# Performance work log

Measured on AMD Instinct MI355X. Metric: run time of the kernel, lower is better.

Reference implementation:

```python
import jax, jax.numpy as jnp
import numpy as np

T, D, H, E = 8192, 1024, 512, 8
BLK = 32  # MXFP8 scaling block size along the contraction dim


def setup_inputs() -> dict:
    key = jax.random.key(0)
    k1, k2, k3, k4 = jax.random.split(key, 4)
    # qdata: values representable-ish in e4m3 (we use small normal floats)
    output_e4m3 = jax.random.normal(k1, (T, D), dtype=jnp.float32)
    # e8m0 scales are powers of two, one per 32-element block along dim
    output_scales_e8m0 = jnp.exp2(
        jax.random.randint(k2, (T, D // BLK), -2, 3).astype(jnp.float32)
    )
    # uniform token distribution across experts (tokens are expert-contiguous)
    num_tokens_per_expert = jnp.full((E,), T // E, dtype=jnp.int32)
    expert_padded_offsets = jnp.zeros((E,), dtype=jnp.int32)  # unused by forward body
    w13 = jax.random.normal(k3, (E, 2 * H, D), dtype=jnp.float32) * 0.02
    w2 = jax.random.normal(k4, (E, D, H), dtype=jnp.float32) * 0.02
    return {
        "output_e4m3": output_e4m3,
        "output_scales_e8m0": output_scales_e8m0,
        "num_tokens_per_expert": num_tokens_per_expert,
        "expert_padded_offsets": expert_padded_offsets,
        "w13": w13,
        "w2": w2,
    }


def reference(output_e4m3, output_scales_e8m0, num_tokens_per_expert,
              expert_padded_offsets, w13, w2):
    # Dequantize MXFP8: qdata * per-block e8m0 scale, blocks of 32 along dim.
    scales = jnp.repeat(output_scales_e8m0, BLK, axis=-1)  # [T, D]
    x = output_e4m3 * scales  # [T, D] high-precision reference activations
    # Grouped GEMM 1: tokens are expert-contiguous with uniform group sizes,
    # so the ragged grouped matmul reduces to a batched einsum per expert.
    tpe = T // E
    xg = x.reshape(E, tpe, D)                       # [E, tpe, D]
    h13 = jnp.einsum("etd,ehd->eth", xg, w13)       # [E, tpe, 2H]
    h1, h3 = h13[..., :H], h13[..., H:]
    h = jax.nn.silu(h1) * h3                        # fused SiLU-gate
    # Grouped GEMM 2
    out = jnp.einsum("eth,edh->etd", h, w2)         # [E, tpe, D]
    return out.reshape(T, D)
```

## Files before the change

### kernel.cpp

```cpp
#include <hip/hip_runtime.h>
#include <hip/hip_bf16.h>

#define T_TOK 8192
#define DDIM  1024
#define HDIM  512
#define NE    8
#define TPE   (T_TOK / NE)

typedef __attribute__((ext_vector_type(4))) float floatx4;
typedef __attribute__((ext_vector_type(8))) short bf16x8;

__device__ __forceinline__ unsigned short f2bf(float f) {
    union { float f; unsigned int u; } v;
    v.f = f;
    unsigned int u = v.u;
    unsigned int r = u + 0x7FFFu + ((u >> 16) & 1u);
    return (unsigned short)(r >> 16);
}

__device__ __forceinline__ unsigned int cvt_pk_bf16(float lo, float hi) {
    unsigned int r;
    asm("v_cvt_pk_bf16_f32 %0, %1, %2" : "=v"(r) : "v"(lo), "v"(hi));
    return r;
}

__device__ __forceinline__ void gld_lds16(const void* g, void* l) {
    __builtin_amdgcn_global_load_lds(
        (const __attribute__((address_space(1))) unsigned int*)g,
        (__attribute__((address_space(3))) unsigned int*)l, 16, 0, 0);
}

__global__ __launch_bounds__(256)
void convert_x_kernel(const float* __restrict__ X, const float* __restrict__ S,
                      unsigned short* __restrict__ Xb)
{
    const int NTX = (T_TOK * DDIM) / 4;
    const int stride = gridDim.x * blockDim.x;
    for (int i = blockIdx.x * blockDim.x + threadIdx.x; i < NTX; i += stride) {
        int row = i >> 8;
        int c4  = i & 255;
        float4 v = reinterpret_cast<const float4*>(X)[i];
        float sc = S[row * (DDIM / 32) + (c4 >> 3)];
        ushort4 b;
        b.x = f2bf(v.x * sc); b.y = f2bf(v.y * sc);
        b.z = f2bf(v.z * sc); b.w = f2bf(v.w * sc);
        reinterpret_cast<ushort4*>(Xb)[i] = b;
    }
}

__device__ __forceinline__ int xcd_swizzle_512(int raw) {
    return (raw & 7) * 64 + (raw >> 3);
}


__global__ __launch_bounds__(256, 2)
void gemm1_silu_kernel(const unsigned short* __restrict__ Xb,
                       const float* __restrict__ W13,
                       __hip_bfloat16* __restrict__ Hout)
{
    const int bid = xcd_swizzle_512(blockIdx.x);
    const int e  = bid >> 6;
    const int mt = (bid >> 3) & 7;
    const int nt = bid & 7;
    const int tok0 = e * TPE + mt * 128;
    const float* __restrict__ We = W13 + (size_t)e * (2 * HDIM) * DDIM;

    __shared__ __hip_bfloat16 sA[2][128][64];
    __shared__ __hip_bfloat16 sB[2][128][64];

    const int tid  = threadIdx.x;
    const int lane = tid & 63;
    const int wave = tid >> 6;
    const int wr = wave >> 1;
    const int wc = wave & 1;
    const int lr = lane & 15;
    const int sw0 = ((lane >> 4) ^ (lane & 7));

    floatx4 acc1[4][2] = {};
    floatx4 acc3[4][2] = {};

    const int srow0 = (tid >> 3);
    const int c8    = (tid & 7) * 8;
    const int dcol  = (tid & 7) * 8;
    const int gcol  = ((tid & 7) ^ (srow0 & 7)) * 8;
    const int swcol = gcol;

    float4 rB0[8], rB1[8];

    auto LOADB = [&](int kk, float4* rB) {
        const int k0 = kk * 64;
        #pragma unroll
        for (int j = 0; j < 4; ++j) {
            int row = srow0 + j * 32;
            int wrow = (j < 2) ? (nt * 64 + row)
                               : (HDIM + nt * 64 + (row - 64));
            const float* p = &We[(size_t)wrow * DDIM + k0 + c8];
            rB[2*j]   = *reinterpret_cast<const float4*>(p);
            rB[2*j+1] = *reinterpret_cast<const float4*>(p + 4);
        }
    };
    auto STAGEA = [&](int kk, int buf) {
        const int k0 = kk * 64;
        #pragma unroll
        for (int j = 0; j < 4; ++j) {
            int row = srow0 + j * 32;
            gld_lds16(&Xb[(size_t)(tok0 + row) * DDIM + k0 + gcol],
                      &sA[buf][row][dcol]);
        }
    };
    auto WRITEB = [&](int buf, const float4* rB) {
        #pragma unroll
        for (int j = 0; j < 4; ++j) {
            int row = srow0 + j * 32;
            uint4 w;
            w.x = cvt_pk_bf16(rB[2*j].x,   rB[2*j].y);
            w.y = cvt_pk_bf16(rB[2*j].z,   rB[2*j].w);
            w.z = cvt_pk_bf16(rB[2*j+1].x, rB[2*j+1].y);
            w.w = cvt_pk_bf16(rB[2*j+1].z, rB[2*j+1].w);
            *reinterpret_cast<uint4*>(&sB[buf][row][swcol]) = w;
        }
    };
    auto COMPUTE = [&](int buf) {
        #pragma unroll
        for (int ks = 0; ks < 2; ++ks) {
            const int rc = (sw0 ^ (ks << 2)) << 3;
            bf16x8 a[4], b1[2], b3[2];
            #pragma unroll
            for (int m = 0; m < 4; ++m)
                a[m] = *reinterpret_cast<const bf16x8*>(&sA[buf][wr * 64 + m * 16 + lr][rc]);
            #pragma unroll
            for (int n = 0; n < 2; ++n) {
                b1[n] = *reinterpret_cast<const bf16x8*>(&sB[buf][wc * 32 + n * 16 + lr][rc]);
                b3[n] = *reinterpret_cast<const bf16x8*>(&sB[buf][64 + wc * 32 + n * 16 + lr][rc]);
            }
            #pragma unroll
            for (int m = 0; m < 4; ++m)
                #pragma unroll
                for (int n = 0; n < 2; ++n) {
                    acc1[m][n] = __builtin_amdgcn_mfma_f32_16x16x32_bf16(a[m], b1[n], acc1[m][n], 0, 0, 0);
                    acc3[m][n] = __builtin_amdgcn_mfma_f32_16x16x32_bf16(a[m], b3[n], acc3[m][n], 0, 0, 0);
                }
        }
    };

    LOADB(0, rB0);
    __builtin_amdgcn_sched_barrier(0);
    LOADB(1, rB1);
    __builtin_amdgcn_sched_barrier(0);
    STAGEA(0, 0);
    __builtin_amdgcn_sched_barrier(0);
    asm volatile("s_waitcnt vmcnt(12)" ::: "memory");
    __builtin_amdgcn_sched_barrier(0);

    for (int t = 0; t < DDIM / 64 - 2; t += 2) {
        WRITEB(0, rB0);
        __builtin_amdgcn_sched_barrier(0);
        LOADB(t + 2, rB0);
        __builtin_amdgcn_sched_barrier(0);
        STAGEA(t + 1, 1);
        __builtin_amdgcn_sched_barrier(0);
        asm volatile("s_waitcnt vmcnt(12) lgkmcnt(0)" ::: "memory");
        __builtin_amdgcn_sched_barrier(0);
        __builtin_amdgcn_s_barrier();
        COMPUTE(0);
        __builtin_amdgcn_s_barrier();
        WRITEB(1, rB1);
        __builtin_amdgcn_sched_barrier(0);
        LOADB(t + 3, rB1);
        __builtin_amdgcn_sched_barrier(0);
        STAGEA(t + 2, 0);
        __builtin_amdgcn_sched_barrier(0);
        asm volatile("s_waitcnt vmcnt(12) lgkmcnt(0)" ::: "memory");
        __builtin_amdgcn_sched_barrier(0);
        __builtin_amdgcn_s_barrier();
        COMPUTE(1);
        __builtin_amdgcn_s_barrier();
    }

    WRITEB(0, rB0);
    __builtin_amdgcn_sched_barrier(0);
    STAGEA(15, 1);
    __builtin_amdgcn_sched_barrier(0);
    asm volatile("s_waitcnt vmcnt(4) lgkmcnt(0)" ::: "memory");
    __builtin_amdgcn_sched_barrier(0);
    __builtin_amdgcn_s_barrier();
    COMPUTE(0);
    __builtin_amdgcn_s_barrier();
    WRITEB(1, rB1);
    __builtin_amdgcn_sched_barrier(0);
    asm volatile("s_waitcnt vmcnt(0) lgkmcnt(0)" ::: "memory");
    __builtin_amdgcn_sched_barrier(0);
    __builtin_amdgcn_s_barrier();
    COMPUTE(1);

    const int hcol0 = nt * 64 + wc * 32;
    #pragma unroll
    for (int m = 0; m < 4; ++m) {
        #pragma unroll
        for (int n = 0; n < 2; ++n) {
            #pragma unroll
            for (int i = 0; i < 4; ++i) {
                int row = tok0 + wr * 64 + m * 16 + (lane >> 4) * 4 + i;
                int col = hcol0 + n * 16 + (lane & 15);
                float h1 = acc1[m][n][i];
                float h3 = acc3[m][n][i];
                float sig = 1.0f / (1.0f + __expf(-h1));
                Hout[(size_t)row * HDIM + col] = __float2bfloat16(h1 * sig * h3);
            }
        }
    }
}

__global__ __launch_bounds__(256, 2)
void gemm2_kernel(const __hip_bfloat16* __restrict__ Hin,
                  const float* __restrict__ W2,
                  float* __restrict__ Out)
{
    const int bid = xcd_swizzle_512(blockIdx.x);
    const int e  = bid >> 6;
    const int nt = (bid >> 3) & 7;
    const int mt = bid & 7;
    const int tok0 = e * TPE + mt * 128;
    const float* __restrict__ We = W2 + (size_t)e * DDIM * HDIM;

    __shared__ __hip_bfloat16 sA[2][128][64];
    __shared__ __hip_bfloat16 sB[2][128][64];

    const int tid  = threadIdx.x;
    const int lane = tid & 63;
    const int wave = tid >> 6;
    const int wr = wave >> 1;
    const int wc = wave & 1;
    const int lr = lane & 15;
    const int sw0 = ((lane >> 4) ^ (lane & 7));

    floatx4 acc[4][4] = {};

    const int srow0 = (tid >> 3);
    const int c8    = (tid & 7) * 8;
    const int dcol  = (tid & 7) * 8;
    const int swcol = ((tid & 7) ^ (srow0 & 7)) * 8;

    float4 rB[8];

    auto LOADB = [&](int kk) {
        const int k0 = kk * 64;
        #pragma unroll
        for (int j = 0; j < 4; ++j) {
            int row = srow0 + j * 32;
            const float* p = &We[(size_t)(nt * 128 + row) * HDIM + k0 + c8];
            rB[2*j]   = *reinterpret_cast<const float4*>(p);
            rB[2*j+1] = *reinterpret_cast<const float4*>(p + 4);
        }
    };
    auto STAGEA = [&](int kk, int buf) {
        const int k0 = kk * 64;
        #pragma unroll
        for (int j = 0; j < 4; ++j) {
            int row = srow0 + j * 32;
            gld_lds16(&Hin[(size_t)(tok0 + row) * HDIM + k0 + swcol],
                      &sA[buf][row][dcol]);
        }
    };
    auto WRITEB = [&](int buf) {
        #pragma unroll
        for (int j = 0; j < 4; ++j) {
            int row = srow0 + j * 32;
            uint4 w;
            w.x = cvt_pk_bf16(rB[2*j].x,   rB[2*j].y);
            w.y = cvt_pk_bf16(rB[2*j].z,   rB[2*j].w);
            w.z = cvt_pk_bf16(rB[2*j+1].x, rB[2*j+1].y);
            w.w = cvt_pk_bf16(rB[2*j+1].z, rB[2*j+1].w);
            *reinterpret_cast<uint4*>(&sB[buf][row][swcol]) = w;
        }
    };
    auto COMPUTE = [&](int buf) {
        #pragma unroll
        for (int ks = 0; ks < 2; ++ks) {
            const int rc = (sw0 ^ (ks << 2)) << 3;
            bf16x8 a[4], b[4];
            #pragma unroll
            for (int m = 0; m < 4; ++m)
                a[m] = *reinterpret_cast<const bf16x8*>(&sA[buf][wr * 64 + m * 16 + lr][rc]);
            #pragma unroll
            for (int n = 0; n < 4; ++n)
                b[n] = *reinterpret_cast<const bf16x8*>(&sB[buf][wc * 64 + n * 16 + lr][rc]);
            #pragma unroll
            for (int m = 0; m < 4; ++m)
                #pragma unroll
                for (int n = 0; n < 4; ++n)
                    acc[m][n] = __builtin_amdgcn_mfma_f32_16x16x32_bf16(a[m], b[n], acc[m][n], 0, 0, 0);
        }
    };

    LOADB(0);
    __builtin_amdgcn_sched_barrier(0);
    STAGEA(0, 0);
    __builtin_amdgcn_sched_barrier(0);
    for (int kk = 0; kk < HDIM / 64 - 1; ++kk) {
        const int buf = kk & 1;
        asm volatile("s_waitcnt vmcnt(4)" ::: "memory");
        __builtin_amdgcn_sched_barrier(0);
        WRITEB(buf);
        __builtin_amdgcn_sched_barrier(0);
        LOADB(kk + 1);
        __builtin_amdgcn_sched_barrier(0);
        STAGEA(kk + 1, buf ^ 1);
        __builtin_amdgcn_sched_barrier(0);
        asm volatile("s_waitcnt vmcnt(12) lgkmcnt(0)" ::: "memory");
        __builtin_amdgcn_sched_barrier(0);
        __builtin_amdgcn_s_barrier();
        COMPUTE(buf);
        __builtin_amdgcn_s_barrier();
    }
    asm volatile("s_waitcnt vmcnt(4)" ::: "memory");
    __builtin_amdgcn_sched_barrier(0);
    WRITEB(1);
    asm volatile("s_waitcnt vmcnt(0) lgkmcnt(0)" ::: "memory");
    __builtin_amdgcn_sched_barrier(0);
    __builtin_amdgcn_s_barrier();
    COMPUTE(1);

    const int dcol0 = nt * 128 + wc * 64;
    #pragma unroll
    for (int m = 0; m < 4; ++m) {
        #pragma unroll
        for (int n = 0; n < 4; ++n) {
            #pragma unroll
            for (int i = 0; i < 4; ++i) {
                int row = tok0 + wr * 64 + m * 16 + (lane >> 4) * 4 + i;
                int col = dcol0 + n * 16 + (lane & 15);
                Out[(size_t)row * DDIM + col] = acc[m][n][i];
            }
        }
    }
}

extern "C" void kernel_launch(void* const* d_in, const int* in_sizes, int n_in,
                              void* d_out, int out_size, void* d_ws, size_t ws_size,
                              hipStream_t stream) {
    const float* X   = (const float*)d_in[0];
    const float* S   = (const float*)d_in[1];
    const float* W13 = (const float*)d_in[4];
    const float* W2  = (const float*)d_in[5];
    float* Out = (float*)d_out;

    __hip_bfloat16* Hb = (__hip_bfloat16*)d_ws;
    unsigned short* Xb = (unsigned short*)d_out;

    convert_x_kernel<<<2048, 256, 0, stream>>>(X, S, Xb);
    gemm1_silu_kernel<<<NE * 8 * 8, 256, 0, stream>>>(Xb, W13, Hb);
    gemm2_kernel<<<NE * 8 * 8, 256, 0, stream>>>(Hb, W2, Out);
}
```

Measured before the change: 56.11 us.

## Restructure GEMM1 main loop to overlap next-tile loads with MFMA compute

```diff
diff --git a/kernel.cpp b/kernel.cpp
--- a/kernel.cpp
+++ b/kernel.cpp
@@ -9,6 +9,8 @@
 
 typedef __attribute__((ext_vector_type(4))) float floatx4;
 typedef __attribute__((ext_vector_type(8))) short bf16x8;
+
+#define SBAR() __builtin_amdgcn_sched_barrier(0)
 
 __device__ __forceinline__ unsigned short f2bf(float f) {
     union { float f; unsigned int u; } v;
@@ -120,78 +122,70 @@
             *reinterpret_cast<uint4*>(&sB[buf][row][swcol]) = w;
         }
     };
-    auto COMPUTE = [&](int buf) {
-        #pragma unroll
-        for (int ks = 0; ks < 2; ++ks) {
-            const int rc = (sw0 ^ (ks << 2)) << 3;
-            bf16x8 a[4], b1[2], b3[2];
-            #pragma unroll
-            for (int m = 0; m < 4; ++m)
-                a[m] = *reinterpret_cast<const bf16x8*>(&sA[buf][wr * 64 + m * 16 + lr][rc]);
+    auto COMPUTE_KS = [&](int buf, int ks) {
+        const int rc = (sw0 ^ (ks << 2)) << 3;
+        bf16x8 a[4], b1[2], b3[2];
+        #pragma unroll
+        for (int m = 0; m < 4; ++m)
+            a[m] = *reinterpret_cast<const bf16x8*>(&sA[buf][wr * 64 + m * 16 + lr][rc]);
+        #pragma unroll
+        for (int n = 0; n < 2; ++n) {
+            b1[n] = *reinterpret_cast<const bf16x8*>(&sB[buf][wc * 32 + n * 16 + lr][rc]);
+            b3[n] = *reinterpret_cast<const bf16x8*>(&sB[buf][64 + wc * 32 + n * 16 + lr][rc]);
+        }
+        #pragma unroll
+        for (int m = 0; m < 4; ++m)
             #pragma unroll
             for (int n = 0; n < 2; ++n) {
-                b1[n] = *reinterpret_cast<const bf16x8*>(&sB[buf][wc * 32 + n * 16 + lr][rc]);
-                b3[n] = *reinterpret_cast<const bf16x8*>(&sB[buf][64 + wc * 32 + n * 16 + lr][rc]);
+                acc1[m][n] = __builtin_amdgcn_mfma_f32_16x16x32_bf16(a[m], b1[n], acc1[m][n], 0, 0, 0);
+                acc3[m][n] = __builtin_amdgcn_mfma_f32_16x16x32_bf16(a[m], b3[n], acc3[m][n], 0, 0, 0);
             }
-            #pragma unroll
-            for (int m = 0; m < 4; ++m)
-                #pragma unroll
-                for (int n = 0; n < 2; ++n) {
-                    acc1[m][n] = __builtin_amdgcn_mfma_f32_16x16x32_bf16(a[m], b1[n], acc1[m][n], 0, 0, 0);
-                    acc3[m][n] = __builtin_amdgcn_mfma_f32_16x16x32_bf16(a[m], b3[n], acc3[m][n], 0, 0, 0);
-                }
-        }
-    };
-
-    LOADB(0, rB0);
-    __builtin_amdgcn_sched_barrier(0);
-    LOADB(1, rB1);
-    __builtin_amdgcn_sched_barrier(0);
-    STAGEA(0, 0);
-    __builtin_amdgcn_sched_barrier(0);
-    asm volatile("s_waitcnt vmcnt(12)" ::: "memory");
-    __builtin_amdgcn_sched_barrier(0);
+    };
+
+    LOADB(0, rB0);  SBAR();
+    STAGEA(0, 0);   SBAR();
+    LOADB(1, rB1);  SBAR();
+    asm volatile("s_waitcnt vmcnt(8)" ::: "memory");
+    SBAR();
+    WRITEB(0, rB0); SBAR();
+    asm volatile("s_waitcnt lgkmcnt(0)" ::: "memory");
+    SBAR();
+    __builtin_amdgcn_s_barrier();
 
     for (int t = 0; t < DDIM / 64 - 2; t += 2) {
-        WRITEB(0, rB0);
-        __builtin_amdgcn_sched_barrier(0);
-        LOADB(t + 2, rB0);
-        __builtin_amdgcn_sched_barrier(0);
-        STAGEA(t + 1, 1);
-        __builtin_amdgcn_sched_barrier(0);
-        asm volatile("s_waitcnt vmcnt(12) lgkmcnt(0)" ::: "memory");
-        __builtin_amdgcn_sched_barrier(0);
+        asm volatile("s_waitcnt vmcnt(0)" ::: "memory");
+        SBAR();
+        WRITEB(1, rB1);     SBAR();
+        STAGEA(t + 1, 1);   SBAR();
+        LOADB(t + 2, rB0);  SBAR();
+        COMPUTE_KS(0, 0);
+        COMPUTE_KS(0, 1);
+        asm volatile("s_waitcnt vmcnt(8)" ::: "memory");
+        SBAR();
         __builtin_amdgcn_s_barrier();
-        COMPUTE(0);
+        asm volatile("s_waitcnt vmcnt(0)" ::: "memory");
+        SBAR();
+        WRITEB(0, rB0);     SBAR();
+        STAGEA(t + 2, 0);   SBAR();
+        LOADB(t + 3, rB1);  SBAR();
+        COMPUTE_KS(1, 0);
+        COMPUTE_KS(1, 1);
+        asm volatile("s_waitcnt vmcnt(8)" ::: "memory");
+        SBAR();
         __builtin_amdgcn_s_barrier();
-        WRITEB(1, rB1);
-        __builtin_amdgcn_sched_barrier(0);
-        LOADB(t + 3, rB1);
-        __builtin_amdgcn_sched_barrier(0);
-        STAGEA(t + 2, 0);
-        __builtin_amdgcn_sched_barrier(0);
-        asm volatile("s_waitcnt vmcnt(12) lgkmcnt(0)" ::: "memory");
-        __builtin_amdgcn_sched_barrier(0);
-        __builtin_amdgcn_s_barrier();
-        COMPUTE(1);
-        __builtin_amdgcn_s_barrier();
-    }
-
-    WRITEB(0, rB0);
-    __builtin_amdgcn_sched_barrier(0);
-    STAGEA(15, 1);
-    __builtin_amdgcn_sched_barrier(0);
-    asm volatile("s_waitcnt vmcnt(4) lgkmcnt(0)" ::: "memory");
-    __builtin_amdgcn_sched_barrier(0);
+    }
+
+    asm volatile("s_waitcnt vmcnt(0)" ::: "memory");
+    SBAR();
+    WRITEB(1, rB1);   SBAR();
+    STAGEA(15, 1);    SBAR();
+    COMPUTE_KS(0, 0);
+    COMPUTE_KS(0, 1);
+    asm volatile("s_waitcnt vmcnt(0)" ::: "memory");
+    SBAR();
     __builtin_amdgcn_s_barrier();
-    COMPUTE(0);
-    __builtin_amdgcn_s_barrier();
-    WRITEB(1, rB1);
-    __builtin_amdgcn_sched_barrier(0);
-    asm volatile("s_waitcnt vmcnt(0) lgkmcnt(0)" ::: "memory");
-    __builtin_amdgcn_sched_barrier(0);
-    __builtin_amdgcn_s_barrier();
-    COMPUTE(1);
+    COMPUTE_KS(1, 0);
+    COMPUTE_KS(1, 1);
 
     const int hcol0 = nt * 64 + wc * 32;
     #pragma unroll
```

After: 55.84 us. About the same (-0.5%).
